# Performance work log

Measured on AMD Instinct MI355X. Metric: run time of the kernel, lower is better.

Reference implementation:

```python
import jax, jax.numpy as jnp
import numpy as np

BETA = 0.95      # LIF membrane decay (init arg)
THR = 1.0        # snntorch Leaky default threshold
NUM_STEPS = 128


@jax.custom_vjp
def spike(x):
    # Heaviside fire with ATan surrogate gradient (snntorch default, alpha=2)
    return (x > 0).astype(x.dtype)

def _spike_fwd(x):
    return spike(x), x

def _spike_bwd(x, g):
    return (g / (1.0 + (jnp.pi * x) ** 2),)

spike.defvjp(_spike_fwd, _spike_bwd)


def setup_inputs() -> dict:
    key = jax.random.key(0)
    ks = jax.random.split(key, 5)
    B, NI, NH, NO = 2048, 1024, 2048, 10
    return {
        "x": jax.random.normal(ks[0], (B, NI), dtype=jnp.float32),
        "w1": jax.random.normal(ks[1], (NH, NI), dtype=jnp.float32) * 0.05,
        "b1": jax.random.normal(ks[2], (NH,), dtype=jnp.float32) * 0.05,
        "w2": jax.random.normal(ks[3], (NO, NH), dtype=jnp.float32) * 0.05,
        "b2": jax.random.normal(ks[4], (NO,), dtype=jnp.float32) * 0.05,
    }


def reference(x, w1, b1, w2, b2):
    # fc1(x) is loop-invariant: compute the input current once.
    cur1 = jnp.einsum("bi,hi->bh", x, w1) + b1  # [B, NH]
    mem1_0 = jnp.zeros_like(cur1)
    mem2_0 = jnp.zeros((x.shape[0], w2.shape[0]), dtype=x.dtype)

    def step(carry, _):
        mem1, mem2 = carry
        # snntorch Leaky, reset-by-subtraction; reset term is detached.
        reset1 = jax.lax.stop_gradient((mem1 > THR).astype(mem1.dtype))
        mem1 = BETA * mem1 + cur1 - reset1 * THR
        spk1 = spike(mem1 - THR)
        cur2 = jnp.einsum("bh,oh->bo", spk1, w2) + b2  # [B, NO]
        reset2 = jax.lax.stop_gradient((mem2 > THR).astype(mem2.dtype))
        mem2 = BETA * mem2 + cur2 - reset2 * THR
        spk2 = spike(mem2 - THR)
        return (mem1, mem2), (spk2, mem2)

    _, (spk2_rec, mem2_rec) = jax.lax.scan(step, (mem1_0, mem2_0), None, length=NUM_STEPS)
    return spk2_rec, mem2_rec  # each [T, B, NO]
```

## Files before the change

### kernel.cpp

```cpp
#include <hip/hip_runtime.h>
#include <hip/hip_bf16.h>


#define B_   2048
#define NI_  1024
#define NH_  2048
#define NO_  10
#define T_   128
#define GB_  8
#define NBLK (B_ / GB_)
#define TC_  32
#define NCH  (T_ / TC_)

typedef __attribute__((ext_vector_type(8))) short short8;
typedef __attribute__((ext_vector_type(4))) float f32x4;
typedef __attribute__((ext_vector_type(4))) unsigned int u32x4;

__device__ __forceinline__ unsigned int bf16_rne(float f) {
  unsigned int u = __float_as_uint(f);
  return (u + 0x7FFFu + ((u >> 16) & 1u)) >> 16;
}

#define G_ASTRIDE 144
#define G_AOFF    0
#define G_BOFF    (128 * G_ASTRIDE)
#define G_SMEM    (2 * 128 * G_ASTRIDE)

__global__ __launch_bounds__(512, 4) void gemm_cur1(
    const float* __restrict__ x, const float* __restrict__ w1,
    const float* __restrict__ b1, float* __restrict__ cur1) {
  __shared__ __align__(16) char smem[G_SMEM];
  const int tid = threadIdx.x;
  const int lane = tid & 63;
  const int wv = tid >> 6;
  const int wm = wv >> 2;
  const int wn = wv & 3;
  const int n15 = lane & 15;
  const int g = lane >> 4;
  const int brow = blockIdx.y * 128;
  const int bcol = blockIdx.x * 128;

  const int r_st = tid >> 3;
  const int kq = tid & 7;

  f32x4 acc[4][2];
#pragma unroll
  for (int tm = 0; tm < 4; ++tm)
#pragma unroll
    for (int tn = 0; tn < 2; ++tn) acc[tm][tn] = f32x4{0, 0, 0, 0};

  for (int kt = 0; kt < NI_; kt += 32) {
#pragma unroll
    for (int p = 0; p < 2; ++p) {
      const int r = r_st + p * 64;
      const float4 va = *reinterpret_cast<const float4*>(
          &x[(size_t)(brow + r) * NI_ + kt + kq * 4]);
      const float4 vb = *reinterpret_cast<const float4*>(
          &w1[(size_t)(bcol + r) * NI_ + kt + kq * 4]);
      const float fa[4] = {va.x, va.y, va.z, va.w};
      const float fb[4] = {vb.x, vb.y, vb.z, vb.w};
      unsigned ha[4], la[4], hb[4], lb[4];
#pragma unroll
      for (int c = 0; c < 4; ++c) {
        ha[c] = bf16_rne(fa[c]);
        la[c] = bf16_rne(fa[c] - __uint_as_float(ha[c] << 16));
        hb[c] = bf16_rne(fb[c]);
        lb[c] = bf16_rne(fb[c] - __uint_as_float(hb[c] << 16));
      }
      char* arow = smem + G_AOFF + r * G_ASTRIDE;
      char* brw  = smem + G_BOFF + r * G_ASTRIDE;
      *reinterpret_cast<uint2*>(arow + kq * 8) =
          uint2{ha[0] | (ha[1] << 16), ha[2] | (ha[3] << 16)};
      *reinterpret_cast<uint2*>(arow + 64 + kq * 8) =
          uint2{la[0] | (la[1] << 16), la[2] | (la[3] << 16)};
      *reinterpret_cast<uint2*>(brw + kq * 8) =
          uint2{hb[0] | (hb[1] << 16), hb[2] | (hb[3] << 16)};
      *reinterpret_cast<uint2*>(brw + 64 + kq * 8) =
          uint2{lb[0] | (lb[1] << 16), lb[2] | (lb[3] << 16)};
    }
    __syncthreads();

    short8 ah[4], al[4], bh2[2], bl2[2];
#pragma unroll
    for (int tm = 0; tm < 4; ++tm) {
      const char* p = smem + G_AOFF + (wm * 64 + tm * 16 + n15) * G_ASTRIDE;
      ah[tm] = *reinterpret_cast<const short8*>(p + g * 16);
      al[tm] = *reinterpret_cast<const short8*>(p + 64 + g * 16);
    }
#pragma unroll
    for (int tn = 0; tn < 2; ++tn) {
      const char* p = smem + G_BOFF + (wn * 32 + tn * 16 + n15) * G_ASTRIDE;
      bh2[tn] = *reinterpret_cast<const short8*>(p + g * 16);
      bl2[tn] = *reinterpret_cast<const short8*>(p + 64 + g * 16);
    }
#pragma unroll
    for (int tm = 0; tm < 4; ++tm)
#pragma unroll
      for (int tn = 0; tn < 2; ++tn) {
        acc[tm][tn] = __builtin_amdgcn_mfma_f32_16x16x32_bf16(
            ah[tm], bh2[tn], acc[tm][tn], 0, 0, 0);
        acc[tm][tn] = __builtin_amdgcn_mfma_f32_16x16x32_bf16(
            ah[tm], bl2[tn], acc[tm][tn], 0, 0, 0);
        acc[tm][tn] = __builtin_amdgcn_mfma_f32_16x16x32_bf16(
            al[tm], bh2[tn], acc[tm][tn], 0, 0, 0);
      }
    __syncthreads();
  }

#pragma unroll
  for (int tn = 0; tn < 2; ++tn) {
    const int col = bcol + wn * 32 + tn * 16 + n15;
    const float bias = b1[col];
#pragma unroll
    for (int tm = 0; tm < 4; ++tm) {
      const int rowb = brow + wm * 64 + tm * 16 + g * 4;
#pragma unroll
      for (int r = 0; r < 4; ++r)
        cur1[(size_t)(rowb + r) * NH_ + col] = acc[tm][tn][r] + bias;
    }
  }
}

#define BITS_OFF 0
#define LUT_OFF  66560
#define COMB_OFF 66688
#define STAG_OFF 148608
#define SMEM_BYTES 158848

__global__ __launch_bounds__(512, 2) void snn_loop(
    const float* __restrict__ cur1, const float* __restrict__ w2,
    const float* __restrict__ b2, float* __restrict__ spk2_rec,
    float* __restrict__ mem2_rec) {
  extern __shared__ char smem[];
  unsigned* bits = reinterpret_cast<unsigned*>(smem + BITS_OFF);
  uint2* lutw = reinterpret_cast<uint2*>(smem + LUT_OFF);
  const uint2* lut = lutw;
  float* comb = reinterpret_cast<float*>(smem + COMB_OFF);
  float* stag = reinterpret_cast<float*>(smem + STAG_OFF);
  const int tid = threadIdx.x;
  const int lane = tid & 63;
  const int w = tid >> 6;
  const int bbase = blockIdx.x * GB_;
  const int bb = bbase + w;

  if (tid < 16) {
    lutw[tid] = uint2{(tid & 1 ? 0x3F80u : 0u) | (tid & 2 ? 0x3F800000u : 0u),
                      (tid & 4 ? 0x3F80u : 0u) | (tid & 8 ? 0x3F800000u : 0u)};
  }

  float mem1[32], c1v[32], spk[32];
  {
    const float* base = cur1 + (size_t)bb * NH_ + lane * 32;
#pragma unroll
    for (int q = 0; q < 8; ++q) {
      const float4 v = *reinterpret_cast<const float4*>(base + q * 4);
      c1v[q * 4 + 0] = v.x; c1v[q * 4 + 1] = v.y;
      c1v[q * 4 + 2] = v.z; c1v[q * 4 + 3] = v.w;
    }
#pragma unroll
    for (int i = 0; i < 32; ++i) { mem1[i] = 0.0f; spk[i] = 0.0f; }
  }

  u32x4 bhi[8], blo[8];
  {
    const int o = lane & 15;
    const int koff = (lane >> 4) * 8;
#pragma unroll
    for (int kbl = 0; kbl < 8; ++kbl) {
      const int kb = w * 8 + kbl;
      unsigned int hw[4], lw[4];
#pragma unroll
      for (int p = 0; p < 4; ++p) {
        unsigned int h0 = 0, h1 = 0, l0 = 0, l1 = 0;
        if (o < NO_) {
          const int k = kb * 32 + koff + p * 2;
          const float f0 = w2[(size_t)o * NH_ + k];
          const float f1 = w2[(size_t)o * NH_ + k + 1];
          h0 = bf16_rne(f0);
          h1 = bf16_rne(f1);
          l0 = bf16_rne(f0 - __uint_as_float(h0 << 16));
          l1 = bf16_rne(f1 - __uint_as_float(h1 << 16));
        }
        hw[p] = h0 | (h1 << 16);
        lw[p] = l0 | (l1 << 16);
      }
      bhi[kbl] = u32x4{hw[0], hw[1], hw[2], hw[3]};
      blo[kbl] = u32x4{lw[0], lw[1], lw[2], lw[3]};
    }
  }

  float mem2 = 0.0f, spk2 = 0.0f, b2v = 0.0f;
  float *srec = nullptr, *mrec = nullptr;
  if (lane < NO_) {
    b2v = b2[lane];
    srec = spk2_rec + (size_t)bb * NO_ + lane;
    mrec = mem2_rec + (size_t)bb * NO_ + lane;
  }

  const int n15 = lane & 15;
  const int g = lane >> 4;

  int rd_off[5], wr_off[5];
#pragma unroll
  for (int j = 0; j < 5; ++j) {
    const int q = lane * 5 + j;
    const int tb = q / 160;
    const int r160 = q - tb * 160;
    const int g2 = r160 / 40;
    const int r40 = r160 - g2 * 40;
    const int n = r40 >> 2;
    const int r = r40 & 3;
    rd_off[j] = w * 320 + q;
    wr_off[j] = (w * TC_ + tb * 16 + g2 * 4 + r) * 10 + n;
  }

  unsigned* bitsw = bits + w * (TC_ * 65) + lane;
  const unsigned char* bytes = reinterpret_cast<const unsigned char*>(smem);

  for (int ch = 0; ch < NCH; ++ch) {
    for (int tl = 0; tl < TC_; ++tl) {
      unsigned W = 0;
#pragma unroll
      for (int i = 31; i >= 0; --i) {
        float m = fmaf(0.95f, mem1[i], c1v[i]);
        m = m - spk[i];
        mem1[i] = m;
        const bool c = m > 1.0f;
        W = W + W + (c ? 1u : 0u);
        spk[i] = c ? 1.0f : 0.0f;
      }
      bitsw[tl * 65] = W;
    }
    __syncthreads();

    for (int b = 0; b < GB_; ++b) {
#pragma unroll
      for (int tb = 0; tb < 2; ++tb) {
        f32x4 acc = {0.0f, 0.0f, 0.0f, 0.0f};
#pragma unroll
        for (int kbl = 0; kbl < 8; ++kbl) {
          const int kb = w * 8 + kbl;
          const unsigned byt =
              bytes[(b * 2080 + tb * 1040 + n15 * 65 + kb) * 4 + g];
          const uint2 lo2 = lut[byt & 15u];
          const uint2 hi2 = lut[byt >> 4];
          const u32x4 A = {lo2.x, lo2.y, hi2.x, hi2.y};
          const short8 af = __builtin_bit_cast(short8, A);
          acc = __builtin_amdgcn_mfma_f32_16x16x32_bf16(
              af, __builtin_bit_cast(short8, bhi[kbl]), acc, 0, 0, 0);
          acc = __builtin_amdgcn_mfma_f32_16x16x32_bf16(
              af, __builtin_bit_cast(short8, blo[kbl]), acc, 0, 0, 0);
        }
        if (n15 < NO_)
          *reinterpret_cast<f32x4*>(
              &comb[w * 2560 + b * 320 + tb * 160 + g * 40 + n15 * 4]) = acc;
      }
    }
    __syncthreads();

#pragma unroll
    for (int j = 0; j < 5; ++j) {
      float s = 0.0f;
#pragma unroll
      for (int ww = 0; ww < 8; ++ww) s += comb[ww * 2560 + rd_off[j]];
      stag[wr_off[j]] = s;
    }

    if (lane < NO_) {
      for (int tl = 0; tl < TC_; ++tl) {
        const float cur2 = stag[(w * TC_ + tl) * 10 + lane] + b2v;
        float m = fmaf(0.95f, mem2, cur2);
        m = m - spk2;
        mem2 = m;
        spk2 = (m > 1.0f) ? 1.0f : 0.0f;
        const int t = ch * TC_ + tl;
        srec[(size_t)t * (B_ * NO_)] = spk2;
        mrec[(size_t)t * (B_ * NO_)] = m;
      }
    }
  }
}

extern "C" void kernel_launch(void* const* d_in, const int* in_sizes, int n_in,
                              void* d_out, int out_size, void* d_ws, size_t ws_size,
                              hipStream_t stream) {
  const float* x  = (const float*)d_in[0];
  const float* w1 = (const float*)d_in[1];
  const float* b1 = (const float*)d_in[2];
  const float* w2 = (const float*)d_in[3];
  const float* b2 = (const float*)d_in[4];
  float* out = (float*)d_out;
  float* cur1 = (float*)d_ws;

  float* spk2_rec = out;
  float* mem2_rec = out + (size_t)T_ * B_ * NO_;

  (void)hipFuncSetAttribute(reinterpret_cast<const void*>(snn_loop),
                            hipFuncAttributeMaxDynamicSharedMemorySize,
                            SMEM_BYTES);

  dim3 g1(NH_ / 128, B_ / 128);
  gemm_cur1<<<g1, 512, 0, stream>>>(x, w1, b1, cur1);
  snn_loop<<<NBLK, 512, SMEM_BYTES, stream>>>(cur1, w2, b2, spk2_rec, mem2_rec);
}
```

Before: 191.6 us.

## Use 256-entry spike LUT, fold reset into precomputed current, drop staging reduction

Result: faster. 185.7 us (-3.0%).

```diff
diff --git a/kernel.cpp b/kernel.cpp
--- a/kernel.cpp
+++ b/kernel.cpp
@@ -26,7 +26,7 @@
 #define G_BOFF    (128 * G_ASTRIDE)
 #define G_SMEM    (2 * 128 * G_ASTRIDE)
 
-__global__ __launch_bounds__(512, 4) void gemm_cur1(
+__global__ __launch_bounds__(512, 2) void gemm_cur1(
     const float* __restrict__ x, const float* __restrict__ w1,
     const float* __restrict__ b1, float* __restrict__ cur1) {
   __shared__ __align__(16) char smem[G_SMEM];
@@ -121,11 +121,10 @@
   }
 }
 
-#define BITS_OFF 0
-#define LUT_OFF  66560
-#define COMB_OFF 66688
-#define STAG_OFF 148608
-#define SMEM_BYTES 158848
+#define LUT_OFF  0
+#define BITS_OFF 4096
+#define COMB_OFF 70656
+#define SMEM_BYTES 152576
 
 __global__ __launch_bounds__(512, 2) void snn_loop(
     const float* __restrict__ cur1, const float* __restrict__ w2,
@@ -133,22 +132,23 @@
     float* __restrict__ mem2_rec) {
   extern __shared__ char smem[];
   unsigned* bits = reinterpret_cast<unsigned*>(smem + BITS_OFF);
-  uint2* lutw = reinterpret_cast<uint2*>(smem + LUT_OFF);
-  const uint2* lut = lutw;
   float* comb = reinterpret_cast<float*>(smem + COMB_OFF);
-  float* stag = reinterpret_cast<float*>(smem + STAG_OFF);
   const int tid = threadIdx.x;
   const int lane = tid & 63;
   const int w = tid >> 6;
   const int bbase = blockIdx.x * GB_;
   const int bb = bbase + w;
 
-  if (tid < 16) {
-    lutw[tid] = uint2{(tid & 1 ? 0x3F80u : 0u) | (tid & 2 ? 0x3F800000u : 0u),
-                      (tid & 4 ? 0x3F80u : 0u) | (tid & 8 ? 0x3F800000u : 0u)};
-  }
-
-  float mem1[32], c1v[32], spk[32];
+  if (tid < 256) {
+    u32x4 e;
+#pragma unroll
+    for (int q = 0; q < 4; ++q)
+      e[q] = ((tid >> (2 * q)) & 1 ? 0x3F80u : 0u) |
+             ((tid >> (2 * q + 1)) & 1 ? 0x3F800000u : 0u);
+    *reinterpret_cast<u32x4*>(smem + LUT_OFF + tid * 16) = e;
+  }
+
+  float mem1[32], c1v[32], c1m[32], cc[32];
   {
     const float* base = cur1 + (size_t)bb * NH_ + lane * 32;
 #pragma unroll
@@ -158,7 +158,11 @@
       c1v[q * 4 + 2] = v.z; c1v[q * 4 + 3] = v.w;
     }
 #pragma unroll
-    for (int i = 0; i < 32; ++i) { mem1[i] = 0.0f; spk[i] = 0.0f; }
+    for (int i = 0; i < 32; ++i) {
+      mem1[i] = 0.0f;
+      c1m[i] = c1v[i] - 1.0f;
+      cc[i] = c1v[i];
+    }
   }
 
   u32x4 bhi[8], blo[8];
@@ -200,21 +204,8 @@
   const int n15 = lane & 15;
   const int g = lane >> 4;
 
-  int rd_off[5], wr_off[5];
-#pragma unroll
-  for (int j = 0; j < 5; ++j) {
-    const int q = lane * 5 + j;
-    const int tb = q / 160;
-    const int r160 = q - tb * 160;
-    const int g2 = r160 / 40;
-    const int r40 = r160 - g2 * 40;
-    const int n = r40 >> 2;
-    const int r = r40 & 3;
-    rd_off[j] = w * 320 + q;
-    wr_off[j] = (w * TC_ + tb * 16 + g2 * 4 + r) * 10 + n;
-  }
-
-  unsigned* bitsw = bits + w * (TC_ * 65) + lane;
+  unsigned* bitsrow = bits + w * 2080 + lane;
+  const int base_bg = BITS_OFF + n15 * 260 + w * 32 + g;
   const unsigned char* bytes = reinterpret_cast<const unsigned char*>(smem);
 
   for (int ch = 0; ch < NCH; ++ch) {
@@ -222,30 +213,26 @@
       unsigned W = 0;
 #pragma unroll
       for (int i = 31; i >= 0; --i) {
-        float m = fmaf(0.95f, mem1[i], c1v[i]);
-        m = m - spk[i];
+        const float m = fmaf(0.95f, mem1[i], cc[i]);
         mem1[i] = m;
         const bool c = m > 1.0f;
         W = W + W + (c ? 1u : 0u);
-        spk[i] = c ? 1.0f : 0.0f;
-      }
-      bitsw[tl * 65] = W;
+        cc[i] = c ? c1m[i] : c1v[i];
+      }
+      bitsrow[tl * 65] = W;
     }
     __syncthreads();
 
     for (int b = 0; b < GB_; ++b) {
 #pragma unroll
       for (int tb = 0; tb < 2; ++tb) {
+        const int rbase = base_bg + b * 8320 + tb * 4160;
         f32x4 acc = {0.0f, 0.0f, 0.0f, 0.0f};
 #pragma unroll
         for (int kbl = 0; kbl < 8; ++kbl) {
-          const int kb = w * 8 + kbl;
-          const unsigned byt =
-              bytes[(b * 2080 + tb * 1040 + n15 * 65 + kb) * 4 + g];
-          const uint2 lo2 = lut[byt & 15u];
-          const uint2 hi2 = lut[byt >> 4];
-          const u32x4 A = {lo2.x, lo2.y, hi2.x, hi2.y};
-          const short8 af = __builtin_bit_cast(short8, A);
+          const unsigned byt = bytes[rbase + kbl * 4];
+          const short8 af = *reinterpret_cast<const short8*>(
+              smem + LUT_OFF + (byt << 4));
           acc = __builtin_amdgcn_mfma_f32_16x16x32_bf16(
               af, __builtin_bit_cast(short8, bhi[kbl]), acc, 0, 0, 0);
           acc = __builtin_amdgcn_mfma_f32_16x16x32_bf16(
@@ -258,17 +245,15 @@
     }
     __syncthreads();
 
-#pragma unroll
-    for (int j = 0; j < 5; ++j) {
-      float s = 0.0f;
-#pragma unroll
-      for (int ww = 0; ww < 8; ++ww) s += comb[ww * 2560 + rd_off[j]];
-      stag[wr_off[j]] = s;
-    }
-
     if (lane < NO_) {
+      const float* cbase = comb + w * 320 + lane * 4;
+#pragma unroll
       for (int tl = 0; tl < TC_; ++tl) {
-        const float cur2 = stag[(w * TC_ + tl) * 10 + lane] + b2v;
+        const int off = (tl >> 4) * 160 + ((tl & 15) >> 2) * 40 + (tl & 3);
+        float s = 0.0f;
+#pragma unroll
+        for (int ww = 0; ww < 8; ++ww) s += cbase[ww * 2560 + off];
+        const float cur2 = s + b2v;
         float m = fmaf(0.95f, mem2, cur2);
         m = m - spk2;
         mem2 = m;
```
